# Performance work log

Measured on AMD Instinct MI355X. Metric: run time of the kernel, lower is better.

The kernel has to match this reference:

```python
import jax, jax.numpy as jnp
import numpy as np

B, N, C = 32, 16384, 256
D, H, S = 64, 128, 7
ITERS = 3
EPS = 1e-6
SCALE = D ** -0.5


def _ln(x, g, b):
    m = jnp.mean(x, axis=-1, keepdims=True)
    v = jnp.var(x, axis=-1, keepdims=True)
    return (x - m) / jnp.sqrt(v + 1e-5) * g + b


def _gru(x, h, Wih, Whh, bih, bhh):
    # PyTorch GRUCell: Wih/Whh are [3D, D]
    gi = x @ Wih.T + bih
    gh = h @ Whh.T + bhh
    ir, iz, inn = jnp.split(gi, 3, axis=-1)
    hr, hz, hn = jnp.split(gh, 3, axis=-1)
    r = jax.nn.sigmoid(ir + hr)
    z = jax.nn.sigmoid(iz + hz)
    n = jnp.tanh(inn + r * hn)
    return (1.0 - z) * n + z * h


def setup_inputs() -> dict:
    key = jax.random.key(0)
    ks = jax.random.split(key, 20)
    s_c = C ** -0.5
    s_d = D ** -0.5
    s_h = H ** -0.5
    p = {}
    p["inputs"] = jax.random.normal(ks[0], (B, N, C), jnp.float32)
    p["slots_mu"] = jax.random.normal(ks[1], (B, S, D), jnp.float32)
    p["ln_in_g"] = jnp.ones((C,), jnp.float32)
    p["ln_in_b"] = jnp.zeros((C,), jnp.float32)
    p["Wk"] = jax.random.normal(ks[2], (C, D), jnp.float32) * s_c
    p["Wv"] = jax.random.normal(ks[3], (C, D), jnp.float32) * s_c
    p["q_ln_g"] = jnp.ones((D,), jnp.float32)
    p["q_ln_b"] = jnp.zeros((D,), jnp.float32)
    p["Wq"] = jax.random.normal(ks[4], (D, D), jnp.float32) * s_d
    p["bq_ln_g"] = jnp.ones((D,), jnp.float32)
    p["bq_ln_b"] = jnp.zeros((D,), jnp.float32)
    p["bWq"] = jax.random.normal(ks[5], (D, D), jnp.float32) * s_d
    p["gru_Wih"] = jax.random.normal(ks[6], (3 * D, D), jnp.float32) * s_d
    p["gru_Whh"] = jax.random.normal(ks[7], (3 * D, D), jnp.float32) * s_d
    p["gru_bih"] = jnp.zeros((3 * D,), jnp.float32)
    p["gru_bhh"] = jnp.zeros((3 * D,), jnp.float32)
    p["mlp_ln_g"] = jnp.ones((D,), jnp.float32)
    p["mlp_ln_b"] = jnp.zeros((D,), jnp.float32)
    p["mlp_W1"] = jax.random.normal(ks[8], (D, H), jnp.float32) * s_d
    p["mlp_b1"] = jnp.zeros((H,), jnp.float32)
    p["mlp_W2"] = jax.random.normal(ks[9], (H, D), jnp.float32) * s_h
    p["mlp_b2"] = jnp.zeros((D,), jnp.float32)
    p["bmlp_ln_g"] = jnp.ones((D,), jnp.float32)
    p["bmlp_ln_b"] = jnp.zeros((D,), jnp.float32)
    p["bmlp_W1"] = jax.random.normal(ks[10], (D, H), jnp.float32) * s_d
    p["bmlp_b1"] = jnp.zeros((H,), jnp.float32)
    p["bmlp_W2"] = jax.random.normal(ks[11], (H, D), jnp.float32) * s_h
    p["bmlp_b2"] = jnp.zeros((D,), jnp.float32)
    return p


def reference(inputs, slots_mu, ln_in_g, ln_in_b, Wk, Wv, q_ln_g, q_ln_b, Wq,
              bq_ln_g, bq_ln_b, bWq, gru_Wih, gru_Whh, gru_bih, gru_bhh,
              mlp_ln_g, mlp_ln_b, mlp_W1, mlp_b1, mlp_W2, mlp_b2,
              bmlp_ln_g, bmlp_ln_b, bmlp_W1, bmlp_b1, bmlp_W2, bmlp_b2):
    x = _ln(inputs, ln_in_g, ln_in_b)          # [B,N,C]
    k = x @ Wk                                  # [B,N,D]
    v = x @ Wv                                  # [B,N,D]
    fg = slots_mu[:, :-1]                       # [B,S-1,D]
    bg = slots_mu[:, -1:]                       # [B,1,D]
    for _ in range(ITERS):
        fg_prev, bg_prev = fg, bg
        fq = _ln(fg, q_ln_g, q_ln_b) @ Wq
        bq = _ln(bg, bq_ln_g, bq_ln_b) @ bWq
        q = jnp.concatenate([fq, bq], axis=1)   # [B,S,D]
        logits = SCALE * jnp.einsum('bnd,bmd->bnm', k, q)  # [B,N,S]
        attn = jax.nn.softmax(logits, axis=-1) + EPS
        fa = attn[..., :-1]
        ba = attn[..., -1:]
        fa = fa / jnp.sum(fa, axis=1, keepdims=True)
        ba = ba / jnp.sum(ba, axis=1, keepdims=True)
        fu = jnp.einsum('bnm,bnd->bmd', fa, v)  # [B,S-1,D]
        bu = jnp.einsum('bnm,bnd->bmd', ba, v)  # [B,1,D]
        fg = _gru(fu.reshape(-1, D), fg_prev.reshape(-1, D),
                  gru_Wih, gru_Whh, gru_bih, gru_bhh).reshape(B, S - 1, D)
        fg = fg + (jax.nn.relu(_ln(fg, mlp_ln_g, mlp_ln_b) @ mlp_W1 + mlp_b1) @ mlp_W2 + mlp_b2)
        # NOTE: original code uses self.gru (shared) for bg, not bg_gru
        bg = _gru(bu.reshape(-1, D), bg_prev.reshape(-1, D),
                  gru_Wih, gru_Whh, gru_bih, gru_bhh).reshape(B, 1, D)
        bg = bg + (jax.nn.relu(_ln(bg, bmlp_ln_g, bmlp_ln_b) @ bmlp_W1 + bmlp_b1) @ bmlp_W2 + bmlp_b2)
    return jnp.concatenate([fg, bg], axis=1)    # [B,S,D]
```

## Files before the change

kernel.cpp:

```cpp
#include <hip/hip_runtime.h>
#include <hip/hip_bf16.h>

typedef __bf16 bf16_t;
typedef __bf16 bf16x4 __attribute__((ext_vector_type(4)));
typedef __bf16 bf16x8 __attribute__((ext_vector_type(8)));
typedef float f32x4 __attribute__((ext_vector_type(4)));

#define B_ 32
#define N_ 16384
#define C_ 256
#define D_ 64
#define ROWS_TOTAL (B_ * N_)

__device__ inline float wave_sum64(float v) {
#pragma unroll
  for (int o = 1; o < 64; o <<= 1) v += __shfl_xor(v, o);
  return v;
}

__device__ inline float sigmoidf_(float x) { return 1.0f / (1.0f + __expf(-x)); }
__device__ inline float tanhf_(float x) { return 1.0f - 2.0f / (__expf(2.0f * x) + 1.0f); }

__global__ __launch_bounds__(256) void prep_kernel(
    const float* __restrict__ Wk, const float* __restrict__ Wv,
    const float* __restrict__ Wih, const float* __restrict__ Whh,
    const float* __restrict__ slots, bf16_t* __restrict__ Wb,
    float* __restrict__ WihT, float* __restrict__ WhhT, float* __restrict__ g) {
  int i = blockIdx.x * 256 + threadIdx.x;
  if (i < 32768) {
    int j = i & 7, l = (i >> 3) & 63, t = (i >> 9) & 7, kb = i >> 12;
    int k = kb * 32 + (l >> 4) * 8 + j;
    int n = t * 16 + (l & 15);
    float v = (n < 64) ? Wk[k * 64 + n] : Wv[k * 64 + (n - 64)];
    Wb[i] = (bf16_t)v;
  } else if (i < 45056) {
    int idx = i - 32768;
    int c = idx / 192, j = idx % 192;
    WihT[idx] = Wih[j * 64 + c];
  } else if (i < 57344) {
    int idx = i - 45056;
    int c = idx / 192, j = idx % 192;
    WhhT[idx] = Whh[j * 64 + c];
  } else if (i < 71680) {
    int idx = i - 57344;
    g[idx] = slots[idx];
  }
}

__global__ __launch_bounds__(512) void proj_ln_kernel(
    const float* __restrict__ inp, const float* __restrict__ lng,
    const float* __restrict__ lnb, const bf16_t* __restrict__ Wb,
    bf16_t* __restrict__ kbuf, bf16_t* __restrict__ vbuf) {
  __shared__ bf16_t xs[128 * 256];
  const int tid = threadIdx.x, w = tid >> 6, lane = tid & 63;
  const int q4 = lane >> 4, lp = lane & 15;
  const long row0 = (long)blockIdx.x * 128;

  float4 gv[4], bv[4];
#pragma unroll
  for (int j = 0; j < 4; ++j) {
    gv[j] = *(const float4*)(lng + lp * 16 + j * 4);
    bv[j] = *(const float4*)(lnb + lp * 16 + j * 4);
  }

#pragma unroll
  for (int i = 0; i < 4; ++i) {
    int r = w * 16 + i * 4 + q4;
    const float* rp = inp + (row0 + r) * C_ + lp * 16;
    float4 x0 = *(const float4*)(rp);
    float4 x1 = *(const float4*)(rp + 4);
    float4 x2 = *(const float4*)(rp + 8);
    float4 x3 = *(const float4*)(rp + 12);
    float s = (x0.x + x0.y + x0.z + x0.w) + (x1.x + x1.y + x1.z + x1.w) +
              (x2.x + x2.y + x2.z + x2.w) + (x3.x + x3.y + x3.z + x3.w);
    float s2 = (x0.x * x0.x + x0.y * x0.y + x0.z * x0.z + x0.w * x0.w) +
               (x1.x * x1.x + x1.y * x1.y + x1.z * x1.z + x1.w * x1.w) +
               (x2.x * x2.x + x2.y * x2.y + x2.z * x2.z + x2.w * x2.w) +
               (x3.x * x3.x + x3.y * x3.y + x3.z * x3.z + x3.w * x3.w);
#pragma unroll
    for (int o = 1; o < 16; o <<= 1) {
      s += __shfl_xor(s, o);
      s2 += __shfl_xor(s2, o);
    }
    float mean = s * (1.0f / 256.0f);
    float var = s2 * (1.0f / 256.0f) - mean * mean;
    float rstd = rsqrtf(var + 1e-5f);
    bf16x8 y0, y1;
    y0[0] = (bf16_t)((x0.x - mean) * rstd * gv[0].x + bv[0].x);
    y0[1] = (bf16_t)((x0.y - mean) * rstd * gv[0].y + bv[0].y);
    y0[2] = (bf16_t)((x0.z - mean) * rstd * gv[0].z + bv[0].z);
    y0[3] = (bf16_t)((x0.w - mean) * rstd * gv[0].w + bv[0].w);
    y0[4] = (bf16_t)((x1.x - mean) * rstd * gv[1].x + bv[1].x);
    y0[5] = (bf16_t)((x1.y - mean) * rstd * gv[1].y + bv[1].y);
    y0[6] = (bf16_t)((x1.z - mean) * rstd * gv[1].z + bv[1].z);
    y0[7] = (bf16_t)((x1.w - mean) * rstd * gv[1].w + bv[1].w);
    y1[0] = (bf16_t)((x2.x - mean) * rstd * gv[2].x + bv[2].x);
    y1[1] = (bf16_t)((x2.y - mean) * rstd * gv[2].y + bv[2].y);
    y1[2] = (bf16_t)((x2.z - mean) * rstd * gv[2].z + bv[2].z);
    y1[3] = (bf16_t)((x2.w - mean) * rstd * gv[2].w + bv[2].w);
    y1[4] = (bf16_t)((x3.x - mean) * rstd * gv[3].x + bv[3].x);
    y1[5] = (bf16_t)((x3.y - mean) * rstd * gv[3].y + bv[3].y);
    y1[6] = (bf16_t)((x3.z - mean) * rstd * gv[3].z + bv[3].z);
    y1[7] = (bf16_t)((x3.w - mean) * rstd * gv[3].w + bv[3].w);
    int base = r * 32, swz = r & 31;
    *(bf16x8*)(xs + (size_t)(base + ((2 * lp) ^ swz)) * 8) = y0;
    *(bf16x8*)(xs + (size_t)(base + ((2 * lp + 1) ^ swz)) * 8) = y1;
  }
  __syncthreads();

  f32x4 acc[8];
  const f32x4 zf = {0.0f, 0.0f, 0.0f, 0.0f};
#pragma unroll
  for (int t = 0; t < 8; ++t) acc[t] = zf;

  const int r0 = w * 16 + lp;
  const int rsw = r0 & 31;
  for (int kb = 0; kb < 8; ++kb) {
    bf16x8 a = *(const bf16x8*)(xs + (size_t)(r0 * 32 + ((kb * 4 + q4) ^ rsw)) * 8);
#pragma unroll
    for (int t = 0; t < 8; ++t) {
      bf16x8 bfr = *(const bf16x8*)(Wb + (size_t)((kb * 8 + t) * 64 + lane) * 8);
      acc[t] = __builtin_amdgcn_mfma_f32_16x16x32_bf16(a, bfr, acc[t], 0, 0, 0);
    }
  }

#pragma unroll
  for (int t = 0; t < 8; ++t) {
    bf16_t* dst = (t < 4) ? kbuf : vbuf;
    int c = (t & 3) * 16 + lp;
#pragma unroll
    for (int reg = 0; reg < 4; ++reg) {
      long gr = row0 + w * 16 + q4 * 4 + reg;
      dst[gr * 64 + c] = (bf16_t)acc[t][reg];
    }
  }
}

__global__ __launch_bounds__(64) void qk_kernel(
    const float* __restrict__ g, const float* __restrict__ qg,
    const float* __restrict__ qb, const float* __restrict__ Wq,
    const float* __restrict__ bqg, const float* __restrict__ bqb,
    const float* __restrict__ bWq, float* __restrict__ q,
    float* __restrict__ acc, float* __restrict__ wsum) {
  __shared__ float sx[64];
  int bid = blockIdx.x, lane = threadIdx.x;
  int m = bid % 7;
  const float* lng = (m < 6) ? qg : bqg;
  const float* lnb = (m < 6) ? qb : bqb;
  const float* W = (m < 6) ? Wq : bWq;
  float gvv = g[bid * 64 + lane];
  float s = wave_sum64(gvv);
  float s2 = wave_sum64(gvv * gvv);
  float mean = s * (1.0f / 64.0f);
  float var = s2 * (1.0f / 64.0f) - mean * mean;
  float rstd = rsqrtf(var + 1e-5f);
  sx[lane] = (gvv - mean) * rstd * lng[lane] + lnb[lane];
  __syncthreads();
  float qd = 0.0f;
#pragma unroll 8
  for (int c = 0; c < 64; ++c) qd += sx[c] * W[c * 64 + lane];
  q[bid * 64 + lane] = qd;
  acc[bid * 64 + lane] = 0.0f;
  if (lane == 0) wsum[bid] = 0.0f;
}

__global__ __launch_bounds__(256) void attend_kernel(
    const bf16_t* __restrict__ kbuf, const bf16_t* __restrict__ vbuf,
    const float* __restrict__ q, float* __restrict__ acc,
    float* __restrict__ wsum) {
  __shared__ float qs[448];
  __shared__ float s_acc[448];
  __shared__ float s_w[7];
  int tid = threadIdx.x, w = tid >> 6, lane = tid & 63;
  int g4 = lane >> 4, lp = lane & 15;
  long chunk0 = (long)blockIdx.x * 512;
  int b = (int)(chunk0 >> 14);

  for (int idx = tid; idx < 448; idx += 256) {
    qs[idx] = q[b * 448 + idx];
    s_acc[idx] = 0.0f;
  }
  if (tid < 7) s_w[tid] = 0.0f;
  __syncthreads();

  float4 qv[7];
  const float4* qs4 = (const float4*)qs;
#pragma unroll
  for (int m = 0; m < 7; ++m) qv[m] = qs4[m * 16 + lp];

  float av[7][4];
  float wa[7];
#pragma unroll
  for (int m = 0; m < 7; ++m) {
    wa[m] = 0.0f;
#pragma unroll
    for (int j = 0; j < 4; ++j) av[m][j] = 0.0f;
  }

  for (int it = 0; it < 32; ++it) {
    long row = chunk0 + it * 16 + w * 4 + g4;
    bf16x4 kv = *(const bf16x4*)(kbuf + row * 64 + lp * 4);
    bf16x4 vv = *(const bf16x4*)(vbuf + row * 64 + lp * 4);
    float k0 = kv[0], k1 = kv[1], k2 = kv[2], k3 = kv[3];
    float lg[7];
#pragma unroll
    for (int m = 0; m < 7; ++m)
      lg[m] = k0 * qv[m].x + k1 * qv[m].y + k2 * qv[m].z + k3 * qv[m].w;
#pragma unroll
    for (int m = 0; m < 7; ++m) {
      lg[m] += __shfl_xor(lg[m], 1);
      lg[m] += __shfl_xor(lg[m], 2);
      lg[m] += __shfl_xor(lg[m], 4);
      lg[m] += __shfl_xor(lg[m], 8);
    }
    float mx = -1e30f;
#pragma unroll
    for (int m = 0; m < 7; ++m) {
      lg[m] *= 0.125f;
      mx = fmaxf(mx, lg[m]);
    }
    float e[7], s = 0.0f;
#pragma unroll
    for (int m = 0; m < 7; ++m) {
      e[m] = __expf(lg[m] - mx);
      s += e[m];
    }
    float inv = 1.0f / s;
    float v0 = vv[0], v1 = vv[1], v2 = vv[2], v3 = vv[3];
#pragma unroll
    for (int m = 0; m < 7; ++m) {
      float a = e[m] * inv + 1e-6f;
      wa[m] += a;
      av[m][0] += a * v0;
      av[m][1] += a * v1;
      av[m][2] += a * v2;
      av[m][3] += a * v3;
    }
  }

#pragma unroll
  for (int m = 0; m < 7; ++m) {
#pragma unroll
    for (int j = 0; j < 4; ++j) {
      av[m][j] += __shfl_xor(av[m][j], 16);
      av[m][j] += __shfl_xor(av[m][j], 32);
    }
    wa[m] += __shfl_xor(wa[m], 16);
    wa[m] += __shfl_xor(wa[m], 32);
  }
  if (g4 == 0) {
#pragma unroll
    for (int m = 0; m < 7; ++m)
#pragma unroll
      for (int j = 0; j < 4; ++j) atomicAdd(&s_acc[m * 64 + lp * 4 + j], av[m][j]);
  }
  if (lane == 0) {
#pragma unroll
    for (int m = 0; m < 7; ++m) atomicAdd(&s_w[m], wa[m]);
  }
  __syncthreads();
  for (int idx = tid; idx < 448; idx += 256) atomicAdd(&acc[b * 448 + idx], s_acc[idx]);
  if (tid < 7) atomicAdd(&wsum[b * 7 + tid], s_w[tid]);
}

__global__ __launch_bounds__(192) void update_kernel(
    const float* __restrict__ acc, const float* __restrict__ wsum,
    const float* __restrict__ g, const float* __restrict__ WihT,
    const float* __restrict__ WhhT, const float* __restrict__ bih,
    const float* __restrict__ bhh, const float* __restrict__ mlg,
    const float* __restrict__ mlb, const float* __restrict__ mW1,
    const float* __restrict__ mb1, const float* __restrict__ mW2,
    const float* __restrict__ mb2, const float* __restrict__ bmlg,
    const float* __restrict__ bmlb, const float* __restrict__ bW1,
    const float* __restrict__ bb1, const float* __restrict__ bW2,
    const float* __restrict__ bb2, float* __restrict__ gout,
    const float* __restrict__ qg, const float* __restrict__ qb,
    const float* __restrict__ Wq, const float* __restrict__ bqg,
    const float* __restrict__ bqb, const float* __restrict__ bWq,
    float* __restrict__ qout, float* __restrict__ accz,
    float* __restrict__ wsz, int write_q) {
  __shared__ float fu[64], hp[64], gi[192], gh[192], h2[64], xb[64], a1[128], go[64];
  int tid = threadIdx.x, bid = blockIdx.x, m = bid % 7;

  const float *lg_, *lb_, *W1_, *b1_, *W2_, *b2_;
  if (m < 6) { lg_ = mlg; lb_ = mlb; W1_ = mW1; b1_ = mb1; W2_ = mW2; b2_ = mb2; }
  else       { lg_ = bmlg; lb_ = bmlb; W1_ = bW1; b1_ = bb1; W2_ = bW2; b2_ = bb2; }

  if (tid < 64) {
    float wv = wsum[bid];
    fu[tid] = acc[bid * 64 + tid] / wv;
    hp[tid] = g[bid * 64 + tid];
  }
  __syncthreads();

  {
    int j = tid;
    float a = bih[j], bsum = bhh[j];
    for (int c = 0; c < 64; ++c) {
      a += fu[c] * WihT[c * 192 + j];
      bsum += hp[c] * WhhT[c * 192 + j];
    }
    gi[j] = a;
    gh[j] = bsum;
  }
  __syncthreads();

  if (tid < 64) {
    int d = tid;
    float r = sigmoidf_(gi[d] + gh[d]);
    float z = sigmoidf_(gi[64 + d] + gh[64 + d]);
    float n = tanhf_(gi[128 + d] + r * gh[128 + d]);
    float h = (1.0f - z) * n + z * hp[d];
    h2[d] = h;
    float s = wave_sum64(h);
    float s2 = wave_sum64(h * h);
    float mean = s * (1.0f / 64.0f);
    float var = s2 * (1.0f / 64.0f) - mean * mean;
    xb[d] = (h - mean) * rsqrtf(var + 1e-5f) * lg_[d] + lb_[d];
  }
  __syncthreads();

  if (tid < 128) {
    int hh = tid;
    float a = b1_[hh];
    for (int c = 0; c < 64; ++c) a += xb[c] * W1_[c * 128 + hh];
    a1[hh] = fmaxf(a, 0.0f);
  }
  __syncthreads();

  if (tid < 64) {
    int d = tid;
    float o = b2_[d];
    for (int hh = 0; hh < 128; ++hh) o += a1[hh] * W2_[hh * 64 + d];
    float res = h2[d] + o;
    gout[bid * 64 + d] = res;
    go[d] = res;
  }
  __syncthreads();

  if (write_q) {
    if (tid < 64) {
      const float* qlng = (m < 6) ? qg : bqg;
      const float* qlnb = (m < 6) ? qb : bqb;
      const float* W = (m < 6) ? Wq : bWq;
      float gvv = go[tid];
      float s = wave_sum64(gvv);
      float s2 = wave_sum64(gvv * gvv);
      float mean = s * (1.0f / 64.0f);
      float var = s2 * (1.0f / 64.0f) - mean * mean;
      xb[tid] = (gvv - mean) * rsqrtf(var + 1e-5f) * qlng[tid] + qlnb[tid];
      __syncwarp();
      float qd = 0.0f;
      const float* Wl = W;
#pragma unroll 8
      for (int c = 0; c < 64; ++c) qd += xb[c] * Wl[c * 64 + tid];
      qout[bid * 64 + tid] = qd;
      accz[bid * 64 + tid] = 0.0f;
      if (tid == 0) wsz[bid] = 0.0f;
    }
  }
}

extern "C" void kernel_launch(void* const* d_in, const int* in_sizes, int n_in,
                              void* d_out, int out_size, void* d_ws, size_t ws_size,
                              hipStream_t stream) {
  const float* inputs   = (const float*)d_in[0];
  const float* slots_mu = (const float*)d_in[1];
  const float* ln_in_g  = (const float*)d_in[2];
  const float* ln_in_b  = (const float*)d_in[3];
  const float* Wk       = (const float*)d_in[4];
  const float* Wv       = (const float*)d_in[5];
  const float* q_ln_g   = (const float*)d_in[6];
  const float* q_ln_b   = (const float*)d_in[7];
  const float* Wq       = (const float*)d_in[8];
  const float* bq_ln_g  = (const float*)d_in[9];
  const float* bq_ln_b  = (const float*)d_in[10];
  const float* bWq      = (const float*)d_in[11];
  const float* gru_Wih  = (const float*)d_in[12];
  const float* gru_Whh  = (const float*)d_in[13];
  const float* gru_bih  = (const float*)d_in[14];
  const float* gru_bhh  = (const float*)d_in[15];
  const float* mlp_ln_g = (const float*)d_in[16];
  const float* mlp_ln_b = (const float*)d_in[17];
  const float* mlp_W1   = (const float*)d_in[18];
  const float* mlp_b1   = (const float*)d_in[19];
  const float* mlp_W2   = (const float*)d_in[20];
  const float* mlp_b2   = (const float*)d_in[21];
  const float* bmlp_ln_g = (const float*)d_in[22];
  const float* bmlp_ln_b = (const float*)d_in[23];
  const float* bmlp_W1  = (const float*)d_in[24];
  const float* bmlp_b1  = (const float*)d_in[25];
  const float* bmlp_W2  = (const float*)d_in[26];
  const float* bmlp_b2  = (const float*)d_in[27];
  float* out = (float*)d_out;

  char* ws = (char*)d_ws;
  const size_t KV_BYTES = (size_t)ROWS_TOTAL * 64 * 2;
  bf16_t* kbuf = (bf16_t*)ws;
  bf16_t* vbuf = (bf16_t*)(ws + KV_BYTES);
  bf16_t* Wb   = (bf16_t*)(ws + 2 * KV_BYTES);
  float* WihT  = (float*)(ws + 2 * KV_BYTES + 65536);
  float* WhhT  = (float*)(ws + 2 * KV_BYTES + 65536 + 49152);
  float* gbuf  = (float*)(ws + 2 * KV_BYTES + 65536 + 2 * 49152);
  float* qbuf  = (float*)(ws + 2 * KV_BYTES + 65536 + 2 * 49152 + 57344);
  float* accb  = (float*)(ws + 2 * KV_BYTES + 65536 + 2 * 49152 + 2 * 57344);
  float* wsumb = (float*)(ws + 2 * KV_BYTES + 65536 + 2 * 49152 + 3 * 57344);

  prep_kernel<<<280, 256, 0, stream>>>(Wk, Wv, gru_Wih, gru_Whh, slots_mu, Wb,
                                       WihT, WhhT, gbuf);
  proj_ln_kernel<<<ROWS_TOTAL / 128, 512, 0, stream>>>(inputs, ln_in_g, ln_in_b,
                                                       Wb, kbuf, vbuf);
  qk_kernel<<<224, 64, 0, stream>>>(gbuf, q_ln_g, q_ln_b, Wq, bq_ln_g, bq_ln_b,
                                    bWq, qbuf, accb, wsumb);
  for (int it = 0; it < 3; ++it) {
    attend_kernel<<<ROWS_TOTAL / 512, 256, 0, stream>>>(kbuf, vbuf, qbuf, accb,
                                                        wsumb);
    update_kernel<<<224, 192, 0, stream>>>(
        accb, wsumb, gbuf, WihT, WhhT, gru_bih, gru_bhh, mlp_ln_g, mlp_ln_b,
        mlp_W1, mlp_b1, mlp_W2, mlp_b2, bmlp_ln_g, bmlp_ln_b, bmlp_W1, bmlp_b1,
        bmlp_W2, bmlp_b2, (it == 2) ? out : gbuf, q_ln_g, q_ln_b, Wq, bq_ln_g,
        bq_ln_b, bWq, qbuf, accb, wsumb, (it < 2) ? 1 : 0);
  }
}
```

Measured before the change: 1.036 ms.

## Fuse attention and slot update via last-block counter; widen proj per-wave tiles

Merges the attention accumulation and GRU/MLP slot update into one kernel: the last block to finish each batch (detected with an atomic counter) performs that batch's update and next query projection. Accumulators, weight sums and counters are given per-iteration copies zeroed once in the prep kernel, removing the separate update launches and re-zeroing. The projection kernel now uses 256 threads with each wave computing two 16-row tiles, reusing each weight fragment for two MFMAs. The tail update is serialized onto one block per batch and the projection change raises register use per thread.

```diff
diff --git a/kernel.cpp b/kernel.cpp
--- a/kernel.cpp
+++ b/kernel.cpp
@@ -18,6 +18,12 @@
   return v;
 }
 
+__device__ inline float half_sum32(float v) {
+#pragma unroll
+  for (int o = 1; o < 32; o <<= 1) v += __shfl_xor(v, o);
+  return v;
+}
+
 __device__ inline float sigmoidf_(float x) { return 1.0f / (1.0f + __expf(-x)); }
 __device__ inline float tanhf_(float x) { return 1.0f - 2.0f / (__expf(2.0f * x) + 1.0f); }
 
@@ -25,7 +31,8 @@
     const float* __restrict__ Wk, const float* __restrict__ Wv,
     const float* __restrict__ Wih, const float* __restrict__ Whh,
     const float* __restrict__ slots, bf16_t* __restrict__ Wb,
-    float* __restrict__ WihT, float* __restrict__ WhhT, float* __restrict__ g) {
+    float* __restrict__ WihT, float* __restrict__ WhhT, float* __restrict__ g,
+    float* __restrict__ accz, float* __restrict__ wsz, int* __restrict__ cnt) {
   int i = blockIdx.x * 256 + threadIdx.x;
   if (i < 32768) {
     int j = i & 7, l = (i >> 3) & 63, t = (i >> 9) & 7, kb = i >> 12;
@@ -44,10 +51,16 @@
   } else if (i < 71680) {
     int idx = i - 57344;
     g[idx] = slots[idx];
-  }
-}
-
-__global__ __launch_bounds__(512) void proj_ln_kernel(
+  } else if (i < 114688) {
+    accz[i - 71680] = 0.0f;
+  } else if (i < 115360) {
+    wsz[i - 114688] = 0.0f;
+  } else if (i < 115456) {
+    cnt[i - 115360] = 0;
+  }
+}
+
+__global__ __launch_bounds__(256) void proj_ln_kernel(
     const float* __restrict__ inp, const float* __restrict__ lng,
     const float* __restrict__ lnb, const bf16_t* __restrict__ Wb,
     bf16_t* __restrict__ kbuf, bf16_t* __restrict__ vbuf) {
@@ -64,8 +77,8 @@
   }
 
 #pragma unroll
-  for (int i = 0; i < 4; ++i) {
-    int r = w * 16 + i * 4 + q4;
+  for (int i = 0; i < 8; ++i) {
+    int r = w * 32 + i * 4 + q4;
     const float* rp = inp + (row0 + r) * C_ + lp * 16;
     float4 x0 = *(const float4*)(rp);
     float4 x1 = *(const float4*)(rp + 4);
@@ -108,30 +121,37 @@
   }
   __syncthreads();
 
-  f32x4 acc[8];
+  f32x4 acc[2][8];
   const f32x4 zf = {0.0f, 0.0f, 0.0f, 0.0f};
 #pragma unroll
-  for (int t = 0; t < 8; ++t) acc[t] = zf;
-
-  const int r0 = w * 16 + lp;
-  const int rsw = r0 & 31;
+  for (int mt = 0; mt < 2; ++mt)
+#pragma unroll
+    for (int t = 0; t < 8; ++t) acc[mt][t] = zf;
+
+  const int r0 = w * 32 + lp, r1 = r0 + 16;
+  const int sw0 = r0 & 31, sw1 = r1 & 31;
   for (int kb = 0; kb < 8; ++kb) {
-    bf16x8 a = *(const bf16x8*)(xs + (size_t)(r0 * 32 + ((kb * 4 + q4) ^ rsw)) * 8);
+    bf16x8 a0 = *(const bf16x8*)(xs + (size_t)(r0 * 32 + ((kb * 4 + q4) ^ sw0)) * 8);
+    bf16x8 a1 = *(const bf16x8*)(xs + (size_t)(r1 * 32 + ((kb * 4 + q4) ^ sw1)) * 8);
 #pragma unroll
     for (int t = 0; t < 8; ++t) {
       bf16x8 bfr = *(const bf16x8*)(Wb + (size_t)((kb * 8 + t) * 64 + lane) * 8);
-      acc[t] = __builtin_amdgcn_mfma_f32_16x16x32_bf16(a, bfr, acc[t], 0, 0, 0);
-    }
-  }
-
-#pragma unroll
-  for (int t = 0; t < 8; ++t) {
-    bf16_t* dst = (t < 4) ? kbuf : vbuf;
-    int c = (t & 3) * 16 + lp;
-#pragma unroll
-    for (int reg = 0; reg < 4; ++reg) {
-      long gr = row0 + w * 16 + q4 * 4 + reg;
-      dst[gr * 64 + c] = (bf16_t)acc[t][reg];
+      acc[0][t] = __builtin_amdgcn_mfma_f32_16x16x32_bf16(a0, bfr, acc[0][t], 0, 0, 0);
+      acc[1][t] = __builtin_amdgcn_mfma_f32_16x16x32_bf16(a1, bfr, acc[1][t], 0, 0, 0);
+    }
+  }
+
+#pragma unroll
+  for (int mt = 0; mt < 2; ++mt) {
+#pragma unroll
+    for (int t = 0; t < 8; ++t) {
+      bf16_t* dst = (t < 4) ? kbuf : vbuf;
+      int c = (t & 3) * 16 + lp;
+#pragma unroll
+      for (int reg = 0; reg < 4; ++reg) {
+        long gr = row0 + w * 32 + mt * 16 + q4 * 4 + reg;
+        dst[gr * 64 + c] = (bf16_t)acc[mt][t][reg];
+      }
     }
   }
 }
@@ -140,8 +160,7 @@
     const float* __restrict__ g, const float* __restrict__ qg,
     const float* __restrict__ qb, const float* __restrict__ Wq,
     const float* __restrict__ bqg, const float* __restrict__ bqb,
-    const float* __restrict__ bWq, float* __restrict__ q,
-    float* __restrict__ acc, float* __restrict__ wsum) {
+    const float* __restrict__ bWq, float* __restrict__ q) {
   __shared__ float sx[64];
   int bid = blockIdx.x, lane = threadIdx.x;
   int m = bid % 7;
@@ -160,111 +179,12 @@
 #pragma unroll 8
   for (int c = 0; c < 64; ++c) qd += sx[c] * W[c * 64 + lane];
   q[bid * 64 + lane] = qd;
-  acc[bid * 64 + lane] = 0.0f;
-  if (lane == 0) wsum[bid] = 0.0f;
-}
-
-__global__ __launch_bounds__(256) void attend_kernel(
+}
+
+__global__ __launch_bounds__(256) void attend_update_kernel(
     const bf16_t* __restrict__ kbuf, const bf16_t* __restrict__ vbuf,
     const float* __restrict__ q, float* __restrict__ acc,
-    float* __restrict__ wsum) {
-  __shared__ float qs[448];
-  __shared__ float s_acc[448];
-  __shared__ float s_w[7];
-  int tid = threadIdx.x, w = tid >> 6, lane = tid & 63;
-  int g4 = lane >> 4, lp = lane & 15;
-  long chunk0 = (long)blockIdx.x * 512;
-  int b = (int)(chunk0 >> 14);
-
-  for (int idx = tid; idx < 448; idx += 256) {
-    qs[idx] = q[b * 448 + idx];
-    s_acc[idx] = 0.0f;
-  }
-  if (tid < 7) s_w[tid] = 0.0f;
-  __syncthreads();
-
-  float4 qv[7];
-  const float4* qs4 = (const float4*)qs;
-#pragma unroll
-  for (int m = 0; m < 7; ++m) qv[m] = qs4[m * 16 + lp];
-
-  float av[7][4];
-  float wa[7];
-#pragma unroll
-  for (int m = 0; m < 7; ++m) {
-    wa[m] = 0.0f;
-#pragma unroll
-    for (int j = 0; j < 4; ++j) av[m][j] = 0.0f;
-  }
-
-  for (int it = 0; it < 32; ++it) {
-    long row = chunk0 + it * 16 + w * 4 + g4;
-    bf16x4 kv = *(const bf16x4*)(kbuf + row * 64 + lp * 4);
-    bf16x4 vv = *(const bf16x4*)(vbuf + row * 64 + lp * 4);
-    float k0 = kv[0], k1 = kv[1], k2 = kv[2], k3 = kv[3];
-    float lg[7];
-#pragma unroll
-    for (int m = 0; m < 7; ++m)
-      lg[m] = k0 * qv[m].x + k1 * qv[m].y + k2 * qv[m].z + k3 * qv[m].w;
-#pragma unroll
-    for (int m = 0; m < 7; ++m) {
-      lg[m] += __shfl_xor(lg[m], 1);
-      lg[m] += __shfl_xor(lg[m], 2);
-      lg[m] += __shfl_xor(lg[m], 4);
-      lg[m] += __shfl_xor(lg[m], 8);
-    }
-    float mx = -1e30f;
-#pragma unroll
-    for (int m = 0; m < 7; ++m) {
-      lg[m] *= 0.125f;
-      mx = fmaxf(mx, lg[m]);
-    }
-    float e[7], s = 0.0f;
-#pragma unroll
-    for (int m = 0; m < 7; ++m) {
-      e[m] = __expf(lg[m] - mx);
-      s += e[m];
-    }
-    float inv = 1.0f / s;
-    float v0 = vv[0], v1 = vv[1], v2 = vv[2], v3 = vv[3];
-#pragma unroll
-    for (int m = 0; m < 7; ++m) {
-      float a = e[m] * inv + 1e-6f;
-      wa[m] += a;
-      av[m][0] += a * v0;
-      av[m][1] += a * v1;
-      av[m][2] += a * v2;
-      av[m][3] += a * v3;
-    }
-  }
-
-#pragma unroll
-  for (int m = 0; m < 7; ++m) {
-#pragma unroll
-    for (int j = 0; j < 4; ++j) {
-      av[m][j] += __shfl_xor(av[m][j], 16);
-      av[m][j] += __shfl_xor(av[m][j], 32);
-    }
-    wa[m] += __shfl_xor(wa[m], 16);
-    wa[m] += __shfl_xor(wa[m], 32);
-  }
-  if (g4 == 0) {
-#pragma unroll
-    for (int m = 0; m < 7; ++m)
-#pragma unroll
-      for (int j = 0; j < 4; ++j) atomicAdd(&s_acc[m * 64 + lp * 4 + j], av[m][j]);
-  }
-  if (lane == 0) {
-#pragma unroll
-    for (int m = 0; m < 7; ++m) atomicAdd(&s_w[m], wa[m]);
-  }
-  __syncthreads();
-  for (int idx = tid; idx < 448; idx += 256) atomicAdd(&acc[b * 448 + idx], s_acc[idx]);
-  if (tid < 7) atomicAdd(&wsum[b * 7 + tid], s_w[tid]);
-}
-
-__global__ __launch_bounds__(192) void update_kernel(
-    const float* __restrict__ acc, const float* __restrict__ wsum,
+    float* __restrict__ wsum, int* __restrict__ cnt,
     const float* __restrict__ g, const float* __restrict__ WihT,
     const float* __restrict__ WhhT, const float* __restrict__ bih,
     const float* __restrict__ bhh, const float* __restrict__ mlg,
@@ -277,86 +197,221 @@
     const float* __restrict__ qg, const float* __restrict__ qb,
     const float* __restrict__ Wq, const float* __restrict__ bqg,
     const float* __restrict__ bqb, const float* __restrict__ bWq,
-    float* __restrict__ qout, float* __restrict__ accz,
-    float* __restrict__ wsz, int write_q) {
-  __shared__ float fu[64], hp[64], gi[192], gh[192], h2[64], xb[64], a1[128], go[64];
-  int tid = threadIdx.x, bid = blockIdx.x, m = bid % 7;
-
-  const float *lg_, *lb_, *W1_, *b1_, *W2_, *b2_;
-  if (m < 6) { lg_ = mlg; lb_ = mlb; W1_ = mW1; b1_ = mb1; W2_ = mW2; b2_ = mb2; }
-  else       { lg_ = bmlg; lb_ = bmlb; W1_ = bW1; b1_ = bb1; W2_ = bW2; b2_ = bb2; }
-
-  if (tid < 64) {
-    float wv = wsum[bid];
-    fu[tid] = acc[bid * 64 + tid] / wv;
-    hp[tid] = g[bid * 64 + tid];
-  }
-  __syncthreads();
-
-  {
-    int j = tid;
-    float a = bih[j], bsum = bhh[j];
-    for (int c = 0; c < 64; ++c) {
-      a += fu[c] * WihT[c * 192 + j];
-      bsum += hp[c] * WhhT[c * 192 + j];
-    }
-    gi[j] = a;
-    gh[j] = bsum;
-  }
-  __syncthreads();
-
-  if (tid < 64) {
-    int d = tid;
-    float r = sigmoidf_(gi[d] + gh[d]);
-    float z = sigmoidf_(gi[64 + d] + gh[64 + d]);
-    float n = tanhf_(gi[128 + d] + r * gh[128 + d]);
-    float h = (1.0f - z) * n + z * hp[d];
-    h2[d] = h;
-    float s = wave_sum64(h);
-    float s2 = wave_sum64(h * h);
+    float* __restrict__ qout, int write_q) {
+  __shared__ float qs[448];
+  __shared__ float s_acc[448];
+  __shared__ float s_w[7];
+  __shared__ int isLast;
+  __shared__ float fuS[7][64], hpS[7][64], giS[7][192], ghS[7][192];
+  __shared__ float xbS[7][64], a1S[7][128];
+
+  int tid = threadIdx.x, w = tid >> 6, lane = tid & 63;
+  int g4 = lane >> 4, lp = lane & 15;
+  long chunk0 = (long)blockIdx.x * 512;
+  int b = (int)(chunk0 >> 14);
+
+  for (int idx = tid; idx < 448; idx += 256) {
+    qs[idx] = q[b * 448 + idx];
+    s_acc[idx] = 0.0f;
+  }
+  if (tid < 7) s_w[tid] = 0.0f;
+  __syncthreads();
+
+  float4 qv[7];
+  const float4* qs4 = (const float4*)qs;
+#pragma unroll
+  for (int m = 0; m < 7; ++m) qv[m] = qs4[m * 16 + lp];
+
+  float av[7][4];
+  float wa[7];
+#pragma unroll
+  for (int m = 0; m < 7; ++m) {
+    wa[m] = 0.0f;
+#pragma unroll
+    for (int j = 0; j < 4; ++j) av[m][j] = 0.0f;
+  }
+
+  for (int it = 0; it < 32; ++it) {
+    long row = chunk0 + it * 16 + w * 4 + g4;
+    bf16x4 kv = *(const bf16x4*)(kbuf + row * 64 + lp * 4);
+    bf16x4 vv = *(const bf16x4*)(vbuf + row * 64 + lp * 4);
+    float k0 = kv[0], k1 = kv[1], k2 = kv[2], k3 = kv[3];
+    float lg[7];
+#pragma unroll
+    for (int m = 0; m < 7; ++m)
+      lg[m] = k0 * qv[m].x + k1 * qv[m].y + k2 * qv[m].z + k3 * qv[m].w;
+#pragma unroll
+    for (int m = 0; m < 7; ++m) {
+      lg[m] += __shfl_xor(lg[m], 1);
+      lg[m] += __shfl_xor(lg[m], 2);
+      lg[m] += __shfl_xor(lg[m], 4);
+      lg[m] += __shfl_xor(lg[m], 8);
+    }
+    float mx = -1e30f;
+#pragma unroll
+    for (int m = 0; m < 7; ++m) {
+      lg[m] *= 0.125f;
+      mx = fmaxf(mx, lg[m]);
+    }
+    float e[7], s = 0.0f;
+#pragma unroll
+    for (int m = 0; m < 7; ++m) {
+      e[m] = __expf(lg[m] - mx);
+      s += e[m];
+    }
+    float inv = 1.0f / s;
+    float v0 = vv[0], v1 = vv[1], v2 = vv[2], v3 = vv[3];
+#pragma unroll
+    for (int m = 0; m < 7; ++m) {
+      float a = e[m] * inv + 1e-6f;
+      wa[m] += a;
+      av[m][0] += a * v0;
+      av[m][1] += a * v1;
+      av[m][2] += a * v2;
+      av[m][3] += a * v3;
+    }
+  }
+
+#pragma unroll
+  for (int m = 0; m < 7; ++m) {
+#pragma unroll
+    for (int j = 0; j < 4; ++j) {
+      av[m][j] += __shfl_xor(av[m][j], 16);
+      av[m][j] += __shfl_xor(av[m][j], 32);
+    }
+    wa[m] += __shfl_xor(wa[m], 16);
+    wa[m] += __shfl_xor(wa[m], 32);
+  }
+  if (g4 == 0) {
+#pragma unroll
+    for (int m = 0; m < 7; ++m)
+#pragma unroll
+      for (int j = 0; j < 4; ++j) atomicAdd(&s_acc[m * 64 + lp * 4 + j], av[m][j]);
+  }
+  if (lane == 0) {
+#pragma unroll
+    for (int m = 0; m < 7; ++m) atomicAdd(&s_w[m], wa[m]);
+  }
+  __syncthreads();
+  for (int idx = tid; idx < 448; idx += 256) atomicAdd(&acc[b * 448 + idx], s_acc[idx]);
+  if (tid < 7) atomicAdd(&wsum[b * 7 + tid], s_w[tid]);
+
+  if (tid == 0) {
+    __threadfence();
+    int old = atomicAdd(&cnt[b], 1);
+    isLast = (old == 31) ? 1 : 0;
+  }
+  __syncthreads();
+  if (!isLast) return;
+  __threadfence();
+
+  int hw = lane >> 5, l32 = lane & 31;
+  int m = w * 2 + hw;
+  bool act = (m < 7);
+  int bid = b * 7 + m;
+  int d0 = l32 * 2, d1 = d0 + 1;
+
+  const float *lg_, *lb_, *W1_, *b1_, *W2_, *b2_, *qlg_, *qlb_, *Wq_;
+  if (m < 6) {
+    lg_ = mlg; lb_ = mlb; W1_ = mW1; b1_ = mb1; W2_ = mW2; b2_ = mb2;
+    qlg_ = qg; qlb_ = qb; Wq_ = Wq;
+  } else {
+    lg_ = bmlg; lb_ = bmlb; W1_ = bW1; b1_ = bb1; W2_ = bW2; b2_ = bb2;
+    qlg_ = bqg; qlb_ = bqb; Wq_ = bWq;
+  }
+
+  if (act) {
+    float wv = __hip_atomic_load(&wsum[bid], __ATOMIC_RELAXED, __HIP_MEMORY_SCOPE_AGENT);
+    float a0 = __hip_atomic_load(&acc[bid * 64 + d0], __ATOMIC_RELAXED, __HIP_MEMORY_SCOPE_AGENT);
+    float a1 = __hip_atomic_load(&acc[bid * 64 + d1], __ATOMIC_RELAXED, __HIP_MEMORY_SCOPE_AGENT);
+    float inv = 1.0f / wv;
+    fuS[m][d0] = a0 * inv;
+    fuS[m][d1] = a1 * inv;
+    hpS[m][d0] = g[bid * 64 + d0];
+    hpS[m][d1] = g[bid * 64 + d1];
+  }
+  __syncthreads();
+
+  if (act) {
+#pragma unroll
+    for (int t = 0; t < 6; ++t) {
+      int j = l32 + 32 * t;
+      float a = bih[j], bs = bhh[j];
+      for (int c = 0; c < 64; ++c) {
+        a += fuS[m][c] * WihT[c * 192 + j];
+        bs += hpS[m][c] * WhhT[c * 192 + j];
+      }
+      giS[m][j] = a;
+      ghS[m][j] = bs;
+    }
+  }
+  __syncthreads();
+
+  float h0 = 0.0f, h1 = 0.0f;
+  if (act) {
+    float r0 = sigmoidf_(giS[m][d0] + ghS[m][d0]);
+    float z0 = sigmoidf_(giS[m][64 + d0] + ghS[m][64 + d0]);
+    float n0 = tanhf_(giS[m][128 + d0] + r0 * ghS[m][128 + d0]);
+    h0 = (1.0f - z0) * n0 + z0 * hpS[m][d0];
+    float r1 = sigmoidf_(giS[m][d1] + ghS[m][d1]);
+    float z1 = sigmoidf_(giS[m][64 + d1] + ghS[m][64 + d1]);
+    float n1 = tanhf_(giS[m][128 + d1] + r1 * ghS[m][128 + d1]);
+    h1 = (1.0f - z1) * n1 + z1 * hpS[m][d1];
+    float s = half_sum32(h0 + h1);
+    float s2 = half_sum32(h0 * h0 + h1 * h1);
     float mean = s * (1.0f / 64.0f);
     float var = s2 * (1.0f / 64.0f) - mean * mean;
-    xb[d] = (h - mean) * rsqrtf(var + 1e-5f) * lg_[d] + lb_[d];
-  }
-  __syncthreads();
-
-  if (tid < 128) {
-    int hh = tid;
-    float a = b1_[hh];
-    for (int c = 0; c < 64; ++c) a += xb[c] * W1_[c * 128 + hh];
-    a1[hh] = fmaxf(a, 0.0f);
-  }
-  __syncthreads();
-
-  if (tid < 64) {
-    int d = tid;
-    float o = b2_[d];
-    for (int hh = 0; hh < 128; ++hh) o += a1[hh] * W2_[hh * 64 + d];
-    float res = h2[d] + o;
-    gout[bid * 64 + d] = res;
-    go[d] = res;
-  }
-  __syncthreads();
+    float rstd = rsqrtf(var + 1e-5f);
+    xbS[m][d0] = (h0 - mean) * rstd * lg_[d0] + lb_[d0];
+    xbS[m][d1] = (h1 - mean) * rstd * lg_[d1] + lb_[d1];
+  }
+  __syncthreads();
+
+  if (act) {
+#pragma unroll
+    for (int t = 0; t < 4; ++t) {
+      int j = l32 + 32 * t;
+      float a = b1_[j];
+      for (int c = 0; c < 64; ++c) a += xbS[m][c] * W1_[c * 128 + j];
+      a1S[m][j] = fmaxf(a, 0.0f);
+    }
+  }
+  __syncthreads();
+
+  float res0 = 0.0f, res1 = 0.0f;
+  if (act) {
+    float o0 = b2_[d0], o1 = b2_[d1];
+    for (int hh = 0; hh < 128; ++hh) {
+      float a = a1S[m][hh];
+      o0 += a * W2_[hh * 64 + d0];
+      o1 += a * W2_[hh * 64 + d1];
+    }
+    res0 = h0 + o0;
+    res1 = h1 + o1;
+    gout[bid * 64 + d0] = res0;
+    gout[bid * 64 + d1] = res1;
+  }
 
   if (write_q) {
-    if (tid < 64) {
-      const float* qlng = (m < 6) ? qg : bqg;
-      const float* qlnb = (m < 6) ? qb : bqb;
-      const float* W = (m < 6) ? Wq : bWq;
-      float gvv = go[tid];
-      float s = wave_sum64(gvv);
-      float s2 = wave_sum64(gvv * gvv);
+    if (act) {
+      float s = half_sum32(res0 + res1);
+      float s2 = half_sum32(res0 * res0 + res1 * res1);
       float mean = s * (1.0f / 64.0f);
       float var = s2 * (1.0f / 64.0f) - mean * mean;
-      xb[tid] = (gvv - mean) * rsqrtf(var + 1e-5f) * qlng[tid] + qlnb[tid];
-      __syncwarp();
-      float qd = 0.0f;
-      const float* Wl = W;
-#pragma unroll 8
-      for (int c = 0; c < 64; ++c) qd += xb[c] * Wl[c * 64 + tid];
-      qout[bid * 64 + tid] = qd;
-      accz[bid * 64 + tid] = 0.0f;
-      if (tid == 0) wsz[bid] = 0.0f;
+      float rstd = rsqrtf(var + 1e-5f);
+      xbS[m][d0] = (res0 - mean) * rstd * qlg_[d0] + qlb_[d0];
+      xbS[m][d1] = (res1 - mean) * rstd * qlg_[d1] + qlb_[d1];
+    }
+    __syncthreads();
+    if (act) {
+      float q0 = 0.0f, q1 = 0.0f;
+      for (int c = 0; c < 64; ++c) {
+        float x = xbS[m][c];
+        q0 += x * Wq_[c * 64 + d0];
+        q1 += x * Wq_[c * 64 + d1];
+      }
+      qout[bid * 64 + d0] = q0;
+      qout[bid * 64 + d1] = q1;
     }
   }
 }
@@ -395,30 +450,31 @@
   float* out = (float*)d_out;
 
   char* ws = (char*)d_ws;
+  size_t off = 0;
   const size_t KV_BYTES = (size_t)ROWS_TOTAL * 64 * 2;
-  bf16_t* kbuf = (bf16_t*)ws;
-  bf16_t* vbuf = (bf16_t*)(ws + KV_BYTES);
-  bf16_t* Wb   = (bf16_t*)(ws + 2 * KV_BYTES);
-  float* WihT  = (float*)(ws + 2 * KV_BYTES + 65536);
-  float* WhhT  = (float*)(ws + 2 * KV_BYTES + 65536 + 49152);
-  float* gbuf  = (float*)(ws + 2 * KV_BYTES + 65536 + 2 * 49152);
-  float* qbuf  = (float*)(ws + 2 * KV_BYTES + 65536 + 2 * 49152 + 57344);
-  float* accb  = (float*)(ws + 2 * KV_BYTES + 65536 + 2 * 49152 + 2 * 57344);
-  float* wsumb = (float*)(ws + 2 * KV_BYTES + 65536 + 2 * 49152 + 3 * 57344);
-
-  prep_kernel<<<280, 256, 0, stream>>>(Wk, Wv, gru_Wih, gru_Whh, slots_mu, Wb,
-                                       WihT, WhhT, gbuf);
-  proj_ln_kernel<<<ROWS_TOTAL / 128, 512, 0, stream>>>(inputs, ln_in_g, ln_in_b,
+  bf16_t* kbuf = (bf16_t*)(ws + off); off += KV_BYTES;
+  bf16_t* vbuf = (bf16_t*)(ws + off); off += KV_BYTES;
+  bf16_t* Wb   = (bf16_t*)(ws + off); off += 65536;
+  float* WihT  = (float*)(ws + off);  off += 49152;
+  float* WhhT  = (float*)(ws + off);  off += 49152;
+  float* gbuf  = (float*)(ws + off);  off += 57344;
+  float* qbuf  = (float*)(ws + off);  off += 57344;
+  float* accb  = (float*)(ws + off);  off += 3 * 14336 * 4;
+  float* wsumb = (float*)(ws + off);  off += 3 * 224 * 4;
+  int*   cntb  = (int*)(ws + off);    off += 3 * 32 * 4;
+
+  prep_kernel<<<451, 256, 0, stream>>>(Wk, Wv, gru_Wih, gru_Whh, slots_mu, Wb,
+                                       WihT, WhhT, gbuf, accb, wsumb, cntb);
+  proj_ln_kernel<<<ROWS_TOTAL / 128, 256, 0, stream>>>(inputs, ln_in_g, ln_in_b,
                                                        Wb, kbuf, vbuf);
   qk_kernel<<<224, 64, 0, stream>>>(gbuf, q_ln_g, q_ln_b, Wq, bq_ln_g, bq_ln_b,
-                                    bWq, qbuf, accb, wsumb);
+                                    bWq, qbuf);
   for (int it = 0; it < 3; ++it) {
-    attend_kernel<<<ROWS_TOTAL / 512, 256, 0, stream>>>(kbuf, vbuf, qbuf, accb,
-                                                        wsumb);
-    update_kernel<<<224, 192, 0, stream>>>(
-        accb, wsumb, gbuf, WihT, WhhT, gru_bih, gru_bhh, mlp_ln_g, mlp_ln_b,
-        mlp_W1, mlp_b1, mlp_W2, mlp_b2, bmlp_ln_g, bmlp_ln_b, bmlp_W1, bmlp_b1,
-        bmlp_W2, bmlp_b2, (it == 2) ? out : gbuf, q_ln_g, q_ln_b, Wq, bq_ln_g,
-        bq_ln_b, bWq, qbuf, accb, wsumb, (it < 2) ? 1 : 0);
-  }
-}
+    attend_update_kernel<<<ROWS_TOTAL / 512, 256, 0, stream>>>(
+        kbuf, vbuf, qbuf, accb + it * 14336, wsumb + it * 224, cntb + it * 32,
+        gbuf, WihT, WhhT, gru_bih, gru_bhh, mlp_ln_g, mlp_ln_b, mlp_W1, mlp_b1,
+        mlp_W2, mlp_b2, bmlp_ln_g, bmlp_ln_b, bmlp_W1, bmlp_b1, bmlp_W2,
+        bmlp_b2, (it == 2) ? out : gbuf, q_ln_g, q_ln_b, Wq, bq_ln_g, bq_ln_b,
+        bWq, qbuf, (it < 2) ? 1 : 0);
+  }
+}
```

Result: slower. 1.698 ms (+64.0%).
